# Kernel optimization log

Measured on AMD Instinct MI355X. Metric: run time of the kernel, lower is better.

## Reference

```python
import jax, jax.numpy as jnp
import numpy as np

N = 32768       # flattened residues (batch*seq)
DIM = 1024      # dim == channel (required by residual add)
NRES = 21       # amino-acid types
RECYCLES = 2


def _quat_to_rot(q):
    w, x, y, z = q[..., 0], q[..., 1], q[..., 2], q[..., 3]
    return jnp.stack([
        jnp.stack([1 - 2 * (y * y + z * z), 2 * (x * y - w * z), 2 * (x * z + w * y)], -1),
        jnp.stack([2 * (x * y + w * z), 1 - 2 * (x * x + z * z), 2 * (y * z - w * x)], -1),
        jnp.stack([2 * (x * z - w * y), 2 * (y * z + w * x), 1 - 2 * (x * x + y * y)], -1),
    ], -2)


def _rand_rigid(key, shape, tscale=1.0):
    # random valid rigid transforms as 4x4 homogeneous matrices
    kq, kt = jax.random.split(key)
    q = jax.random.normal(kq, shape + (4,), jnp.float32)
    q = q / jnp.linalg.norm(q, axis=-1, keepdims=True)
    rot = _quat_to_rot(q)
    t = jax.random.normal(kt, shape + (3,), jnp.float32) * tscale
    m = jnp.zeros(shape + (4, 4), jnp.float32)
    m = m.at[..., :3, :3].set(rot).at[..., :3, 3].set(t).at[..., 3, 3].set(1.0)
    return m


def setup_inputs():
    key = jax.random.key(0)
    ks = jax.random.split(key, 12)
    s = 1.0 / np.sqrt(DIM)
    return {
        "rep0": jax.random.normal(ks[0], (N, DIM), jnp.float32),
        "rep1": jax.random.normal(ks[1], (N, DIM), jnp.float32),
        "w_in": jax.random.normal(ks[2], (DIM, DIM), jnp.float32) * s,
        "b_in": jnp.zeros((DIM,), jnp.float32),
        "w1": jax.random.normal(ks[3], (DIM, DIM), jnp.float32) * s,
        "b1": jnp.zeros((DIM,), jnp.float32),
        "w2": jax.random.normal(ks[4], (DIM, DIM), jnp.float32) * s,
        "b2": jnp.zeros((DIM,), jnp.float32),
        "w_ang": jax.random.normal(ks[5], (DIM, 14), jnp.float32) * s,
        "b_ang": jnp.zeros((14,), jnp.float32),
        "rigids": _rand_rigid(ks[6], (N,), tscale=10.0),              # backbone frames
        "default_frames": _rand_rigid(ks[7], (NRES, 8), tscale=1.5), # restype_rigid_group_default_frame
        "lit_positions": jax.random.normal(ks[8], (NRES, 14, 3), jnp.float32),
        "atom_mask": (jax.random.uniform(ks[9], (NRES, 14)) > 0.2).astype(jnp.float32),
        "aatype": jax.random.randint(ks[10], (N,), 0, NRES),
        "group_idx": jax.random.randint(ks[11], (NRES, 14), 0, 8),   # restype_atom14_to_rigid_group
    }


def reference(rep0, rep1, w_in, b_in, w1, b1, w2, b2, w_ang, b_ang,
              rigids, default_frames, lit_positions, atom_mask, aatype, group_idx):
    # InputProjection: shared ReLU+Linear applied to each representation, summed
    act = (jax.nn.relu(rep0) @ w_in + b_in) + (jax.nn.relu(rep1) @ w_in + b_in)
    # ResidueBlock with residual recycles: act += Linear(ReLU(Linear(ReLU(act))))
    for _ in range(RECYCLES):
        h = jax.nn.relu(act) @ w1 + b1
        h = jax.nn.relu(h) @ w2 + b2
        act = act + h
    # TorisonAngles: Linear(dim,14) -> (N,7,2) -> l2_normalize
    ang = (jax.nn.relu(act) @ w_ang + b_ang).reshape(N, 7, 2)
    angles = ang / jnp.sqrt(jnp.maximum(jnp.sum(ang * ang, -1, keepdims=True), 1e-12))
    # torsion_angles_to_frames: prepend identity backbone angle (sin=0, cos=1)
    sin = jnp.concatenate([jnp.zeros((N, 1), angles.dtype), angles[..., 0]], 1)  # [N,8]
    cos = jnp.concatenate([jnp.ones((N, 1), angles.dtype), angles[..., 1]], 1)
    z = jnp.zeros_like(sin); one = jnp.ones_like(sin)
    rotx = jnp.stack([
        jnp.stack([one, z, z, z], -1),
        jnp.stack([z, cos, -sin, z], -1),
        jnp.stack([z, sin, cos, z], -1),
        jnp.stack([z, z, z, one], -1),
    ], -2)                                            # [N,8,4,4] rotation about x by torsion
    frames = default_frames[aatype] @ rotx            # [N,8,4,4]
    # chi2/chi3/chi4 frames are defined relative to the previous chi frame
    f5 = frames[:, 4] @ frames[:, 5]
    f6 = f5 @ frames[:, 6]
    f7 = f6 @ frames[:, 7]
    frames_to_bb = jnp.concatenate([frames[:, :5], jnp.stack([f5, f6, f7], 1)], 1)
    frames_global = rigids[:, None] @ frames_to_bb    # [N,8,4,4]
    # frames_and_literature_positions_to_atom14_pos
    gidx = group_idx[aatype]                          # [N,14] rigid-group id per atom
    f14 = jnp.take_along_axis(frames_global,
                              jnp.broadcast_to(gidx[:, :, None, None], (N, 14, 4, 4)),
                              axis=1)                 # [N,14,4,4]
    pos = lit_positions[aatype]                       # [N,14,3]
    pred = jnp.einsum('naij,naj->nai', f14[..., :3, :3], pos) + f14[..., :3, 3]
    pred = pred * atom_mask[aatype][..., None]        # [N,14,3]
    return angles, pred, frames_global
```

## Files before the change

### kernel.cpp

```cpp
#include <hip/hip_runtime.h>
#include <stdint.h>

typedef uint16_t u16;
typedef uint32_t u32;
typedef __bf16 bf16;
typedef bf16 bf16x8 __attribute__((ext_vector_type(8)));
typedef float f32x4 __attribute__((ext_vector_type(4)));

#define N_RES 32768
#define DIM 1024

__device__ __forceinline__ float b2f(u16 u) {
  u32 v = ((u32)u) << 16;
  float f;
  __builtin_memcpy(&f, &v, 4);
  return f;
}
__device__ __forceinline__ u16 f2b(float f) {
  u32 u;
  __builtin_memcpy(&u, &f, 4);
  u += 0x7fffu + ((u >> 16) & 1u);
  return (u16)(u >> 16);
}
__device__ __forceinline__ void split2(float v, u16& h, u16& l) {
  h = f2b(v);
  l = f2b(v - b2f(h));
}
__device__ __forceinline__ void relu_mask4(uint4& h, uint4& l) {
  u32 s, m;
  s = h.x & 0x80008000u; m = ((s >> 15) & 0x00010001u) * 0xFFFFu; h.x &= ~m; l.x &= ~m;
  s = h.y & 0x80008000u; m = ((s >> 15) & 0x00010001u) * 0xFFFFu; h.y &= ~m; l.y &= ~m;
  s = h.z & 0x80008000u; m = ((s >> 15) & 0x00010001u) * 0xFFFFu; h.z &= ~m; l.z &= ~m;
  s = h.w & 0x80008000u; m = ((s >> 15) & 0x00010001u) * 0xFFFFu; h.w &= ~m; l.w &= ~m;
}
__device__ __forceinline__ void relu_split8(bf16x8& h, bf16x8& l) {
  uint4 uh, ul;
  __builtin_memcpy(&uh, &h, 16);
  __builtin_memcpy(&ul, &l, 16);
  relu_mask4(uh, ul);
  __builtin_memcpy(&h, &uh, 16);
  __builtin_memcpy(&l, &ul, 16);
}
__device__ __forceinline__ void split8(const float* v, uint4& H, uint4& L) {
  u16 h[8], l[8];
#pragma unroll
  for (int i = 0; i < 8; ++i) split2(v[i], h[i], l[i]);
  H.x = (u32)h[0] | ((u32)h[1] << 16);
  H.y = (u32)h[2] | ((u32)h[3] << 16);
  H.z = (u32)h[4] | ((u32)h[5] << 16);
  H.w = (u32)h[6] | ((u32)h[7] << 16);
  L.x = (u32)l[0] | ((u32)l[1] << 16);
  L.y = (u32)l[2] | ((u32)l[3] << 16);
  L.z = (u32)l[4] | ((u32)l[5] << 16);
  L.w = (u32)l[6] | ((u32)l[7] << 16);
}

__device__ __forceinline__ void g2l16(const void* g, void* lds) {
  __builtin_amdgcn_global_load_lds(
      (__attribute__((address_space(1))) void*)(g),
      (__attribute__((address_space(3))) void*)(lds), 16, 0, 0);
}

__global__ __launch_bounds__(256) void transpose_split(const float* __restrict__ in,
                                                       u16* __restrict__ outh,
                                                       u16* __restrict__ outl) {
  __shared__ float t[32][33];
  const int bx = blockIdx.x * 32, by = blockIdx.y * 32;
  const int tx = threadIdx.x, ty = threadIdx.y;
  for (int i = ty; i < 32; i += 8) t[i][tx] = in[(size_t)(by + i) * DIM + bx + tx];
  __syncthreads();
  for (int i = ty; i < 32; i += 8) {
    u16 h, l;
    split2(t[tx][i], h, l);
    const size_t o = (size_t)(bx + i) * DIM + by + tx;
    outh[o] = h;
    outl[o] = l;
  }
}

__global__ __launch_bounds__(256) void prep_input(const float* __restrict__ rep0,
                                                  const float* __restrict__ rep1,
                                                  u16* __restrict__ oh,
                                                  u16* __restrict__ ol) {
  const size_t base = ((size_t)blockIdx.x * 256 + threadIdx.x) * 8;
  float4 x0 = *(const float4*)(rep0 + base);
  float4 x1 = *(const float4*)(rep0 + base + 4);
  float4 y0 = *(const float4*)(rep1 + base);
  float4 y1 = *(const float4*)(rep1 + base + 4);
  float v[8];
  v[0] = fmaxf(x0.x, 0.f) + fmaxf(y0.x, 0.f);
  v[1] = fmaxf(x0.y, 0.f) + fmaxf(y0.y, 0.f);
  v[2] = fmaxf(x0.z, 0.f) + fmaxf(y0.z, 0.f);
  v[3] = fmaxf(x0.w, 0.f) + fmaxf(y0.w, 0.f);
  v[4] = fmaxf(x1.x, 0.f) + fmaxf(y1.x, 0.f);
  v[5] = fmaxf(x1.y, 0.f) + fmaxf(y1.y, 0.f);
  v[6] = fmaxf(x1.z, 0.f) + fmaxf(y1.z, 0.f);
  v[7] = fmaxf(x1.w, 0.f) + fmaxf(y1.w, 0.f);
  uint4 H, L;
  split8(v, H, L);
  *(uint4*)(oh + base) = H;
  *(uint4*)(ol + base) = L;
}

__global__ __launch_bounds__(256, 2) void gemm_split(
    const u16* __restrict__ Ah, const u16* __restrict__ Al, int reluA,
    const u16* __restrict__ Bh, const u16* __restrict__ Bl,
    const float* __restrict__ bias, float bscale,
    const u16* __restrict__ Rh, const u16* __restrict__ Rl,
    u16* __restrict__ Oh, u16* __restrict__ Ol) {
  __shared__ __align__(16) u16 AS[2][128 * 64];
  __shared__ __align__(16) u16 BS[2][128 * 64];
  const int tid = threadIdx.x;
  const int wave = tid >> 6;
  const int lane = tid & 63;
  const int lrow = lane & 15;
  const int lquad = lane >> 4;

  const int g = blockIdx.x + (blockIdx.y << 3);
  const int xcd = g & 7;
  const int j = g >> 3;
  const int bm = (xcd * 32 + (j >> 3)) * 128;
  const int bn = (j & 7) * 128;

  const int wm = (wave & 1) * 64;
  const int wn = (wave >> 1) * 64;

  f32x4 acc[4][4];
#pragma unroll
  for (int i = 0; i < 4; ++i)
#pragma unroll
    for (int jj = 0; jj < 4; ++jj) acc[i][jj] = (f32x4){0.f, 0.f, 0.f, 0.f};

  const int srow = tid >> 3;
  const int dc = (tid & 7) ^ (srow & 7);
  const size_t scol = (size_t)(dc & 3) * 8;
  const u16* srcA = ((dc < 4) ? Ah : Al) + (size_t)(bm + srow) * DIM + scol;
  const u16* srcB = ((dc < 4) ? Bh : Bl) + (size_t)(bn + srow) * DIM + scol;
  u16* dA0 = &AS[0][0] + tid * 8;
  u16* dA1 = &AS[1][0] + tid * 8;
  u16* dB0 = &BS[0][0] + tid * 8;
  u16* dB1 = &BS[1][0] + tid * 8;

  const int swzH = ((lquad ^ (lrow & 7)) * 8);
  const int swzL = swzH ^ 32;

#define STAGE(BUFA, BUFB, KT)                                        \
  {                                                                  \
    const size_t ko = (size_t)(KT) * 32;                             \
    _Pragma("unroll") for (int is = 0; is < 4; ++is) {               \
      g2l16(srcA + ko + (size_t)is * 32 * DIM, (BUFA) + is * 2048);  \
      g2l16(srcB + ko + (size_t)is * 32 * DIM, (BUFB) + is * 2048);  \
    }                                                                \
  }

  STAGE(dA0, dB0, 0);
  __syncthreads();

  int cur = 0;
  for (int kt = 0; kt < 32; ++kt) {
    if (kt + 1 < 32) {
      if (cur == 0) {
        STAGE(dA1, dB1, kt + 1);
      } else {
        STAGE(dA0, dB0, kt + 1);
      }
    }

    const u16* As = &AS[cur][0];
    const u16* Bs = &BS[cur][0];
    bf16x8 a_h[4], a_l[4], b_h[4], b_l[4];
#pragma unroll
    for (int i = 0; i < 4; ++i) {
      const u16* arow = As + (wm + i * 16 + lrow) * 64;
      a_h[i] = *(const bf16x8*)(arow + swzH);
      a_l[i] = *(const bf16x8*)(arow + swzL);
      if (reluA) relu_split8(a_h[i], a_l[i]);
    }
#pragma unroll
    for (int jj = 0; jj < 4; ++jj) {
      const u16* brow = Bs + (wn + jj * 16 + lrow) * 64;
      b_h[jj] = *(const bf16x8*)(brow + swzH);
      b_l[jj] = *(const bf16x8*)(brow + swzL);
    }
#pragma unroll
    for (int i = 0; i < 4; ++i)
#pragma unroll
      for (int jj = 0; jj < 4; ++jj) {
        acc[i][jj] = __builtin_amdgcn_mfma_f32_16x16x32_bf16(a_h[i], b_h[jj], acc[i][jj], 0, 0, 0);
        acc[i][jj] = __builtin_amdgcn_mfma_f32_16x16x32_bf16(a_h[i], b_l[jj], acc[i][jj], 0, 0, 0);
        acc[i][jj] = __builtin_amdgcn_mfma_f32_16x16x32_bf16(a_l[i], b_h[jj], acc[i][jj], 0, 0, 0);
      }
    __syncthreads();
    cur ^= 1;
  }
#undef STAGE

#pragma unroll
  for (int jj = 0; jj < 4; ++jj) {
    const int col = bn + wn + jj * 16 + lrow;
    const float bj = bias[col] * bscale;
#pragma unroll
    for (int i = 0; i < 4; ++i) {
      const int row0 = bm + wm + i * 16 + lquad * 4;
#pragma unroll
      for (int r = 0; r < 4; ++r) {
        const size_t idx = (size_t)(row0 + r) * DIM + col;
        float v = acc[i][jj][r] + bj;
        if (Rh) v += b2f(Rh[idx]) + b2f(Rl[idx]);
        u16 h, l;
        split2(v, h, l);
        Oh[idx] = h;
        Ol[idx] = l;
      }
    }
  }
}

__global__ __launch_bounds__(256) void angles_split(
    const u16* __restrict__ ACTh, const u16* __restrict__ ACTl,
    const u16* __restrict__ WAh, const u16* __restrict__ WAl,
    const float* __restrict__ b_ang, float* __restrict__ out_angles) {
  const int tid = threadIdx.x;
  const int wave = tid >> 6, lane = tid & 63;
  const int lrow = lane & 15, lquad = lane >> 4;
  const int rowA = blockIdx.x * 64 + wave * 16 + lrow;
  f32x4 acc = (f32x4){0.f, 0.f, 0.f, 0.f};
  const u16* gah = ACTh + (size_t)rowA * DIM + lquad * 8;
  const u16* gal = ACTl + (size_t)rowA * DIM + lquad * 8;
  const u16* gbh = WAh + (size_t)lrow * DIM + lquad * 8;
  const u16* gbl = WAl + (size_t)lrow * DIM + lquad * 8;
#pragma unroll 4
  for (int kb = 0; kb < DIM; kb += 32) {
    bf16x8 ah = *(const bf16x8*)(gah + kb);
    bf16x8 al = *(const bf16x8*)(gal + kb);
    relu_split8(ah, al);
    bf16x8 bh = *(const bf16x8*)(gbh + kb);
    bf16x8 bl = *(const bf16x8*)(gbl + kb);
    acc = __builtin_amdgcn_mfma_f32_16x16x32_bf16(ah, bh, acc, 0, 0, 0);
    acc = __builtin_amdgcn_mfma_f32_16x16x32_bf16(ah, bl, acc, 0, 0, 0);
    acc = __builtin_amdgcn_mfma_f32_16x16x32_bf16(al, bh, acc, 0, 0, 0);
  }
  const int col = lrow;
  const float bj = (col < 14) ? b_ang[col] : 0.f;
#pragma unroll
  for (int r = 0; r < 4; ++r) {
    float v = acc[r] + bj;
    float p = __shfl_xor(v, 1, 64);
    float s2 = fmaxf(v * v + p * p, 1e-12f);
    float o = v * rsqrtf(s2);
    const int orow = blockIdx.x * 64 + wave * 16 + lquad * 4 + r;
    if (col < 14) out_angles[(size_t)orow * 14 + col] = o;
  }
}

__global__ __launch_bounds__(256) void prep_wang(const float* __restrict__ w,
                                                 u16* __restrict__ outh,
                                                 u16* __restrict__ outl) {
  for (int idx = threadIdx.x; idx < 16 * 1024; idx += 256) {
    const int n = idx & 15;
    const int k = idx >> 4;
    const float v = (n < 14) ? w[(size_t)k * 14 + n] : 0.f;
    u16 h, l;
    split2(v, h, l);
    outh[(size_t)n * DIM + k] = h;
    outl[(size_t)n * DIM + k] = l;
  }
}

__device__ __forceinline__ void mm34(const float* A, const float* B, float* O) {
#pragma unroll
  for (int r = 0; r < 3; ++r) {
#pragma unroll
    for (int c = 0; c < 4; ++c) {
      float v = A[r * 4 + 0] * B[0 * 4 + c] + A[r * 4 + 1] * B[1 * 4 + c] +
                A[r * 4 + 2] * B[2 * 4 + c];
      if (c == 3) v += A[r * 4 + 3];
      O[r * 4 + c] = v;
    }
  }
}

__global__ __launch_bounds__(256) void frames_kernel(
    const float* __restrict__ angles, const float* __restrict__ rigids,
    const float* __restrict__ dframes, const float* __restrict__ litpos,
    const float* __restrict__ amask, const int* __restrict__ aatype,
    const int* __restrict__ gidx, float* __restrict__ out_pred,
    float* __restrict__ out_frames) {
  const int n = blockIdx.x * 256 + threadIdx.x;
  const int aa = aatype[n];

  float fr[8][12];
  const float* angp = angles + (size_t)n * 14;
#pragma unroll
  for (int g = 0; g < 8; ++g) {
    float s, c;
    if (g == 0) { s = 0.f; c = 1.f; }
    else { s = angp[(g - 1) * 2]; c = angp[(g - 1) * 2 + 1]; }
    const float* D = dframes + ((size_t)aa * 8 + g) * 16;
#pragma unroll
    for (int r = 0; r < 3; ++r) {
      float d0 = D[r * 4 + 0], d1 = D[r * 4 + 1], d2 = D[r * 4 + 2], d3 = D[r * 4 + 3];
      fr[g][r * 4 + 0] = d0;
      fr[g][r * 4 + 1] = d1 * c + d2 * s;
      fr[g][r * 4 + 2] = d2 * c - d1 * s;
      fr[g][r * 4 + 3] = d3;
    }
  }
  float tmp[12];
  mm34(fr[4], fr[5], tmp);
#pragma unroll
  for (int e = 0; e < 12; ++e) fr[5][e] = tmp[e];
  mm34(fr[5], fr[6], tmp);
#pragma unroll
  for (int e = 0; e < 12; ++e) fr[6][e] = tmp[e];
  mm34(fr[6], fr[7], tmp);
#pragma unroll
  for (int e = 0; e < 12; ++e) fr[7][e] = tmp[e];

  float R[12];
  const float* rp = rigids + (size_t)n * 16;
#pragma unroll
  for (int e = 0; e < 12; ++e) R[e] = rp[e];
#pragma unroll
  for (int g = 0; g < 8; ++g) {
    mm34(R, fr[g], tmp);
#pragma unroll
    for (int e = 0; e < 12; ++e) fr[g][e] = tmp[e];
  }

  float4* of = (float4*)(out_frames + (size_t)n * 128);
#pragma unroll
  for (int g = 0; g < 8; ++g) {
    of[g * 4 + 0] = (float4){fr[g][0], fr[g][1], fr[g][2], fr[g][3]};
    of[g * 4 + 1] = (float4){fr[g][4], fr[g][5], fr[g][6], fr[g][7]};
    of[g * 4 + 2] = (float4){fr[g][8], fr[g][9], fr[g][10], fr[g][11]};
    of[g * 4 + 3] = (float4){0.f, 0.f, 0.f, 1.f};
  }

  float P[42];
#pragma unroll
  for (int a = 0; a < 14; ++a) {
    const int g = gidx[aa * 14 + a];
    float f[12];
#pragma unroll
    for (int q = 0; q < 8; ++q) {
      if (q == 0) {
#pragma unroll
        for (int e = 0; e < 12; ++e) f[e] = fr[0][e];
      } else {
        const bool sel = (g == q);
#pragma unroll
        for (int e = 0; e < 12; ++e) f[e] = sel ? fr[q][e] : f[e];
      }
    }
    const float px = litpos[((size_t)aa * 14 + a) * 3 + 0];
    const float py = litpos[((size_t)aa * 14 + a) * 3 + 1];
    const float pz = litpos[((size_t)aa * 14 + a) * 3 + 2];
    const float mk = amask[aa * 14 + a];
    P[a * 3 + 0] = (f[0] * px + f[1] * py + f[2] * pz + f[3]) * mk;
    P[a * 3 + 1] = (f[4] * px + f[5] * py + f[6] * pz + f[7]) * mk;
    P[a * 3 + 2] = (f[8] * px + f[9] * py + f[10] * pz + f[11]) * mk;
  }
  float2* op = (float2*)(out_pred + (size_t)n * 42);
#pragma unroll
  for (int i = 0; i < 21; ++i) op[i] = (float2){P[2 * i], P[2 * i + 1]};
}

__global__ __launch_bounds__(256) void ws_diag(float* __restrict__ out, float mb) {
  const int i = blockIdx.x * 256 + threadIdx.x;
  if (i < N_RES * 14) out[i] = mb;
}

extern "C" void kernel_launch(void* const* d_in, const int* in_sizes, int n_in,
                              void* d_out, int out_size, void* d_ws, size_t ws_size,
                              hipStream_t stream) {
  const float* rep0 = (const float*)d_in[0];
  const float* rep1 = (const float*)d_in[1];
  const float* w_in = (const float*)d_in[2];
  const float* b_in = (const float*)d_in[3];
  const float* w1 = (const float*)d_in[4];
  const float* b1 = (const float*)d_in[5];
  const float* w2 = (const float*)d_in[6];
  const float* b2 = (const float*)d_in[7];
  const float* w_ang = (const float*)d_in[8];
  const float* b_ang = (const float*)d_in[9];
  const float* rigids = (const float*)d_in[10];
  const float* dframes = (const float*)d_in[11];
  const float* litpos = (const float*)d_in[12];
  const float* amask = (const float*)d_in[13];
  const int* aatype = (const int*)d_in[14];
  const int* gidx = (const int*)d_in[15];

  const size_t SLOT = (size_t)N_RES * DIM;
  const size_t NEED_U16 = 4 * SLOT + 6 * (size_t)DIM * DIM + 2 * 16 * DIM;

  float* out_ang = (float*)d_out;
  float* out_pred = out_ang + (size_t)N_RES * 14;
  float* out_frames = out_pred + (size_t)N_RES * 42;

  if (ws_size < NEED_U16 * 2) {
    ws_diag<<<(N_RES * 14 + 255) / 256, 256, 0, stream>>>(
        out_ang, (float)(ws_size >> 20));
    return;
  }

  u16* ACTh = (u16*)d_ws;
  u16* ACTl = ACTh + SLOT;
  u16* Hh = ACTl + SLOT;
  u16* Hl = Hh + SLOT;
  u16* W0h = Hl + SLOT;
  u16* W0l = W0h + (size_t)DIM * DIM;
  u16* W1h = W0l + (size_t)DIM * DIM;
  u16* W1l = W1h + (size_t)DIM * DIM;
  u16* W2h = W1l + (size_t)DIM * DIM;
  u16* W2l = W2h + (size_t)DIM * DIM;
  u16* WAh = W2l + (size_t)DIM * DIM;
  u16* WAl = WAh + (size_t)16 * DIM;

  transpose_split<<<dim3(32, 32), dim3(32, 8), 0, stream>>>(w_in, W0h, W0l);
  transpose_split<<<dim3(32, 32), dim3(32, 8), 0, stream>>>(w1, W1h, W1l);
  transpose_split<<<dim3(32, 32), dim3(32, 8), 0, stream>>>(w2, W2h, W2l);
  prep_wang<<<1, 256, 0, stream>>>(w_ang, WAh, WAl);

  prep_input<<<(N_RES * DIM / 8) / 256, 256, 0, stream>>>(rep0, rep1, Hh, Hl);

  dim3 gg(DIM / 128, N_RES / 128);
  gemm_split<<<gg, 256, 0, stream>>>(Hh, Hl, 0, W0h, W0l, b_in, 2.f,
                                     nullptr, nullptr, ACTh, ACTl);
  gemm_split<<<gg, 256, 0, stream>>>(ACTh, ACTl, 1, W1h, W1l, b1, 1.f,
                                     nullptr, nullptr, Hh, Hl);
  gemm_split<<<gg, 256, 0, stream>>>(Hh, Hl, 1, W2h, W2l, b2, 1.f,
                                     ACTh, ACTl, ACTh, ACTl);
  gemm_split<<<gg, 256, 0, stream>>>(ACTh, ACTl, 1, W1h, W1l, b1, 1.f,
                                     nullptr, nullptr, Hh, Hl);
  gemm_split<<<gg, 256, 0, stream>>>(Hh, Hl, 1, W2h, W2l, b2, 1.f,
                                     ACTh, ACTl, ACTh, ACTl);

  angles_split<<<N_RES / 64, 256, 0, stream>>>(ACTh, ACTl, WAh, WAl, b_ang,
                                               out_ang);
  frames_kernel<<<N_RES / 256, 256, 0, stream>>>(out_ang, rigids, dframes, litpos,
                                                 amask, aatype, gidx, out_pred,
                                                 out_frames);
}
```

Measured before the change: 1.783 ms.

## Single-buffer GEMM LDS for higher occupancy and stage epilogue through LDS

Removes the double-buffered LDS prefetch in the split-bf16 GEMM and uses one shared buffer, cutting LDS per block in half. Launch bounds rise from 2 to 4 blocks per CU, so more waves can hide memory latency instead of explicit prefetch. The epilogue now writes the packed hi/lo results into swizzled LDS and then does coalesced 16-byte global stores and residual loads, replacing scattered 2-byte accesses. The risk is that load/compute overlap within a block is lost, extra barriers are added, and register pressure under the tighter launch bound may cause spills.

```diff
diff --git a/kernel.cpp b/kernel.cpp
--- a/kernel.cpp
+++ b/kernel.cpp
@@ -102,14 +102,17 @@
   *(uint4*)(ol + base) = L;
 }
 
-__global__ __launch_bounds__(256, 2) void gemm_split(
+__global__ __launch_bounds__(256, 4) void gemm_split(
     const u16* __restrict__ Ah, const u16* __restrict__ Al, int reluA,
     const u16* __restrict__ Bh, const u16* __restrict__ Bl,
     const float* __restrict__ bias, float bscale,
     const u16* __restrict__ Rh, const u16* __restrict__ Rl,
     u16* __restrict__ Oh, u16* __restrict__ Ol) {
-  __shared__ __align__(16) u16 AS[2][128 * 64];
-  __shared__ __align__(16) u16 BS[2][128 * 64];
+  __shared__ __align__(16) u32 SMEM[8192];
+  u16* AS = (u16*)SMEM;
+  u16* BS = (u16*)SMEM + 8192;
+  u32* C_lds = SMEM;
+
   const int tid = threadIdx.x;
   const int wave = tid >> 6;
   const int lane = tid & 63;
@@ -136,49 +139,32 @@
   const size_t scol = (size_t)(dc & 3) * 8;
   const u16* srcA = ((dc < 4) ? Ah : Al) + (size_t)(bm + srow) * DIM + scol;
   const u16* srcB = ((dc < 4) ? Bh : Bl) + (size_t)(bn + srow) * DIM + scol;
-  u16* dA0 = &AS[0][0] + tid * 8;
-  u16* dA1 = &AS[1][0] + tid * 8;
-  u16* dB0 = &BS[0][0] + tid * 8;
-  u16* dB1 = &BS[1][0] + tid * 8;
+  u16* dA = AS + (size_t)tid * 8;
+  u16* dB = BS + (size_t)tid * 8;
 
   const int swzH = ((lquad ^ (lrow & 7)) * 8);
   const int swzL = swzH ^ 32;
 
-#define STAGE(BUFA, BUFB, KT)                                        \
-  {                                                                  \
-    const size_t ko = (size_t)(KT) * 32;                             \
-    _Pragma("unroll") for (int is = 0; is < 4; ++is) {               \
-      g2l16(srcA + ko + (size_t)is * 32 * DIM, (BUFA) + is * 2048);  \
-      g2l16(srcB + ko + (size_t)is * 32 * DIM, (BUFB) + is * 2048);  \
-    }                                                                \
-  }
-
-  STAGE(dA0, dB0, 0);
-  __syncthreads();
-
-  int cur = 0;
   for (int kt = 0; kt < 32; ++kt) {
-    if (kt + 1 < 32) {
-      if (cur == 0) {
-        STAGE(dA1, dB1, kt + 1);
-      } else {
-        STAGE(dA0, dB0, kt + 1);
-      }
-    }
-
-    const u16* As = &AS[cur][0];
-    const u16* Bs = &BS[cur][0];
+    const size_t ko = (size_t)kt * 32;
+#pragma unroll
+    for (int is = 0; is < 4; ++is) {
+      g2l16(srcA + ko + (size_t)is * 32 * DIM, dA + is * 2048);
+      g2l16(srcB + ko + (size_t)is * 32 * DIM, dB + is * 2048);
+    }
+    __syncthreads();
+
     bf16x8 a_h[4], a_l[4], b_h[4], b_l[4];
 #pragma unroll
     for (int i = 0; i < 4; ++i) {
-      const u16* arow = As + (wm + i * 16 + lrow) * 64;
+      const u16* arow = AS + (wm + i * 16 + lrow) * 64;
       a_h[i] = *(const bf16x8*)(arow + swzH);
       a_l[i] = *(const bf16x8*)(arow + swzL);
       if (reluA) relu_split8(a_h[i], a_l[i]);
     }
 #pragma unroll
     for (int jj = 0; jj < 4; ++jj) {
-      const u16* brow = Bs + (wn + jj * 16 + lrow) * 64;
+      const u16* brow = BS + (wn + jj * 16 + lrow) * 64;
       b_h[jj] = *(const bf16x8*)(brow + swzH);
       b_l[jj] = *(const bf16x8*)(brow + swzL);
     }
@@ -191,28 +177,68 @@
         acc[i][jj] = __builtin_amdgcn_mfma_f32_16x16x32_bf16(a_l[i], b_h[jj], acc[i][jj], 0, 0, 0);
       }
     __syncthreads();
-    cur ^= 1;
-  }
-#undef STAGE
-
-#pragma unroll
-  for (int jj = 0; jj < 4; ++jj) {
-    const int col = bn + wn + jj * 16 + lrow;
-    const float bj = bias[col] * bscale;
-#pragma unroll
-    for (int i = 0; i < 4; ++i) {
-      const int row0 = bm + wm + i * 16 + lquad * 4;
-#pragma unroll
-      for (int r = 0; r < 4; ++r) {
-        const size_t idx = (size_t)(row0 + r) * DIM + col;
-        float v = acc[i][jj][r] + bj;
-        if (Rh) v += b2f(Rh[idx]) + b2f(Rl[idx]);
-        u16 h, l;
-        split2(v, h, l);
-        Oh[idx] = h;
-        Ol[idx] = l;
+  }
+
+#pragma unroll
+  for (int half = 0; half < 2; ++half) {
+    if (wm == half * 64) {
+#pragma unroll
+      for (int jj = 0; jj < 4; ++jj) {
+        const int colL = wn + jj * 16 + lrow;
+        const float bj = bias[bn + colL] * bscale;
+#pragma unroll
+        for (int i = 0; i < 4; ++i) {
+#pragma unroll
+          for (int r = 0; r < 4; ++r) {
+            const int row = i * 16 + lquad * 4 + r;
+            u16 h, l;
+            split2(acc[i][jj][r] + bj, h, l);
+            C_lds[row * 128 + (colL ^ ((row & 7) << 2))] = (u32)h | ((u32)l << 16);
+          }
+        }
       }
     }
+    __syncthreads();
+    {
+      const int r64 = tid & 63;
+      const int wv = tid >> 6;
+      const int grow = bm + half * 64 + r64;
+      const int swz = (r64 & 7) << 2;
+      const u32* crow = C_lds + r64 * 128;
+      const size_t gbase = (size_t)grow * DIM + bn + wv * 32;
+#pragma unroll
+      for (int g2 = 0; g2 < 4; ++g2) {
+        const int cb = wv * 32 + g2 * 8;
+        uint4 qa = *(const uint4*)&crow[cb ^ swz];
+        uint4 qb = *(const uint4*)&crow[(cb + 4) ^ swz];
+        float v[8];
+        v[0] = b2f((u16)(qa.x & 0xFFFF)) + b2f((u16)(qa.x >> 16));
+        v[1] = b2f((u16)(qa.y & 0xFFFF)) + b2f((u16)(qa.y >> 16));
+        v[2] = b2f((u16)(qa.z & 0xFFFF)) + b2f((u16)(qa.z >> 16));
+        v[3] = b2f((u16)(qa.w & 0xFFFF)) + b2f((u16)(qa.w >> 16));
+        v[4] = b2f((u16)(qb.x & 0xFFFF)) + b2f((u16)(qb.x >> 16));
+        v[5] = b2f((u16)(qb.y & 0xFFFF)) + b2f((u16)(qb.y >> 16));
+        v[6] = b2f((u16)(qb.z & 0xFFFF)) + b2f((u16)(qb.z >> 16));
+        v[7] = b2f((u16)(qb.w & 0xFFFF)) + b2f((u16)(qb.w >> 16));
+        if (Rh) {
+          uint4 rh = *(const uint4*)(Rh + gbase + g2 * 8);
+          uint4 rl = *(const uint4*)(Rl + gbase + g2 * 8);
+          v[0] += b2f((u16)(rh.x & 0xFFFF)) + b2f((u16)(rl.x & 0xFFFF));
+          v[1] += b2f((u16)(rh.x >> 16)) + b2f((u16)(rl.x >> 16));
+          v[2] += b2f((u16)(rh.y & 0xFFFF)) + b2f((u16)(rl.y & 0xFFFF));
+          v[3] += b2f((u16)(rh.y >> 16)) + b2f((u16)(rl.y >> 16));
+          v[4] += b2f((u16)(rh.z & 0xFFFF)) + b2f((u16)(rl.z & 0xFFFF));
+          v[5] += b2f((u16)(rh.z >> 16)) + b2f((u16)(rl.z >> 16));
+          v[6] += b2f((u16)(rh.w & 0xFFFF)) + b2f((u16)(rl.w & 0xFFFF));
+          v[7] += b2f((u16)(rh.w >> 16)) + b2f((u16)(rl.w >> 16));
+        }
+        uint4 H, L;
+        split8(v, H, L);
+        *(uint4*)(Oh + gbase + g2 * 8) = H;
+        *(uint4*)(Ol + gbase + g2 * 8) = L;
+      }
+    }
+    __syncthreads();
   }
 }
 
```

Result: slower. 3.410 ms (+91.3%).
